# Kernel tuning notes

Hardware: AMD Instinct MI355X
Metric: run time of the kernel (lower is better)

Reference implementation:

```python
import jax, jax.numpy as jnp
import numpy as np

N_STREAMS = 8
DIM = 1024
N_HEADS = 16
HEAD_DIM = DIM // N_HEADS
STREAM_DIM = DIM // N_STREAMS
EPS = 1e-6


def setup_inputs() -> dict:
    key = jax.random.key(0)
    ks = jax.random.split(key, 20)
    B, S, D = 2, 2048, DIM
    inp = {
        "x": jax.random.normal(ks[0], (B, S, D), jnp.float32),
        "rope_cos": jax.random.uniform(ks[1], (S, HEAD_DIM), jnp.float32),
        "rope_sin": jax.random.uniform(ks[2], (S, HEAD_DIM), jnp.float32),
        # DeltaOperator: learned per-channel decay logits
        "delta_decay": jax.random.normal(ks[3], (D,), jnp.float32) * 0.02,
        # gate_proj: Linear(D, 3*n)
        "gate_w": jax.random.normal(ks[4], (3 * N_STREAMS, D), jnp.float32) * 0.02,
        "gate_b": jnp.zeros((3 * N_STREAMS,), jnp.float32),
        "phi_res": jax.random.normal(ks[5], (N_STREAMS, N_STREAMS), jnp.float32) * 0.02,
        "ln1_w": jnp.ones((D,), jnp.float32),
        "ln2_w": jnp.ones((D,), jnp.float32),
        # MLP (StrategicLinear == Linear at inference)
        "w1": jax.random.normal(ks[6], (4 * D, D), jnp.float32) * 0.02,
        "b1": jnp.zeros((4 * D,), jnp.float32),
        "w2": jax.random.normal(ks[7], (D, 4 * D), jnp.float32) * 0.02,
        "b2": jnp.zeros((D,), jnp.float32),
        # nn.MultiheadAttention params
        "in_proj_w": jax.random.normal(ks[8], (3 * D, D), jnp.float32) * 0.02,
        "in_proj_b": jnp.zeros((3 * D,), jnp.float32),
        "out_w": jax.random.normal(ks[9], (D, D), jnp.float32) * 0.02,
        "out_b": jnp.zeros((D,), jnp.float32),
    }
    return inp


def delta_operator(x, decay_logits):
    # out_t = x_t - s_{t-1};  s_t = beta*s_{t-1} + (1-beta)*x_t  (per-channel EMA delta)
    beta = jax.nn.sigmoid(decay_logits)  # [D]

    def step(s, xt):
        out = xt - s
        s_new = beta * s + (1.0 - beta) * xt
        return s_new, out

    xT = jnp.swapaxes(x, 0, 1)  # [S,B,D]
    s0 = jnp.zeros_like(xT[0])
    _, ysT = jax.lax.scan(step, s0, xT)
    return jnp.swapaxes(ysT, 0, 1)  # [B,S,D]


def rms_norm(x, w):
    var = jnp.mean(x * x, axis=-1, keepdims=True)
    return x * jax.lax.rsqrt(var + EPS) * w


def sinkhorn_knopp(phi, iterations=15):
    K = jnp.exp(phi)
    for _ in range(iterations):
        K = K / jnp.sum(K, axis=1, keepdims=True)
        K = K / jnp.sum(K, axis=0, keepdims=True)
    return K


def causal_mha(x, in_proj_w, in_proj_b, out_w, out_b):
    B, S, D = x.shape
    qkv = x @ in_proj_w.T + in_proj_b  # [B,S,3D]
    q, k, v = jnp.split(qkv, 3, axis=-1)
    def heads(t):
        return t.reshape(B, S, N_HEADS, HEAD_DIM).transpose(0, 2, 1, 3)  # [B,H,S,hd]
    q, k, v = heads(q), heads(k), heads(v)
    scores = jnp.einsum("bhqd,bhkd->bhqk", q, k) / jnp.sqrt(jnp.float32(HEAD_DIM))
    mask = jnp.tril(jnp.ones((S, S), bool))
    scores = jnp.where(mask, scores, jnp.float32(-1e9))
    attn = jax.nn.softmax(scores, axis=-1)
    o = jnp.einsum("bhqk,bhkd->bhqd", attn, v)
    o = o.transpose(0, 2, 1, 3).reshape(B, S, D)
    return o @ out_w.T + out_b


def reference(x, rope_cos, rope_sin, delta_decay, gate_w, gate_b, phi_res,
              ln1_w, ln2_w, w1, b1, w2, b2, in_proj_w, in_proj_b, out_w, out_b):
    B, S, D = x.shape
    n = N_STREAMS
    x_delta = delta_operator(x, delta_decay)
    x_state = jnp.mean(x_delta, axis=1)  # [B,D]
    gates = x_state @ gate_w.T + gate_b  # [B,3n]
    g_res = jax.nn.sigmoid(gates[:, 2 * n:])[:, None, :, None]  # [B,1,n,1]
    H_res = sinkhorn_knopp(phi_res, 15)
    x_streams = x_delta.reshape(B, S, n, STREAM_DIM)
    # (x_perm @ H.T).permute back == einsum over stream axis
    mhc_out = jnp.einsum("bsnd,mn->bsmd", x_streams * g_res, H_res).reshape(B, S, D)
    normed = rms_norm(x_delta, ln1_w)
    attn_out = causal_mha(normed, in_proj_w, in_proj_b, out_w, out_b)
    normed2 = rms_norm(x_delta + attn_out, ln2_w)
    h = jax.nn.gelu(normed2 @ w1.T + b1, approximate=False)
    ffn_out = h @ w2.T + b2
    return x_delta + attn_out + ffn_out + mhc_out
```

## Files before the change

kernel.cpp:

```cpp
#include <hip/hip_runtime.h>
#include <hip/hip_bf16.h>
#include <math.h>

#define BB 2
#define SS 2048
#define DDIM 1024
#define NHEAD 16
#define NSTR 8
#define SDIMC 128
#define NCH 16
#define CLEN 128
#define EPSV 1e-6f

using bf16 = __hip_bfloat16;
typedef __attribute__((ext_vector_type(8))) __bf16 bf8;
typedef __attribute__((ext_vector_type(4))) float f4;

__device__ __forceinline__ bf16 f2b(float v) { return __float2bfloat16(v); }
__device__ __forceinline__ bf8 ld8(const bf16* p) { return *(const bf8*)p; }
__device__ __forceinline__ f4 MFMA(bf8 a, bf8 b, f4 c) {
  return __builtin_amdgcn_mfma_f32_16x16x32_bf16(a, b, c, 0, 0, 0);
}
__device__ __forceinline__ float sigm(float x) { return 1.0f / (1.0f + expf(-x)); }
__device__ __forceinline__ float fexp2(float x) { return __builtin_amdgcn_exp2f(x); }

__device__ __forceinline__ void glds16(bf16* l, const bf16* g) {
  __builtin_amdgcn_global_load_lds(
      (const __attribute__((address_space(1))) unsigned int*)g,
      (__attribute__((address_space(3))) unsigned int*)l, 16, 0, 0);
}

__global__ __launch_bounds__(256) void cvt_all(const float* __restrict__ ipw,
                                               const float* __restrict__ ow,
                                               const float* __restrict__ w1,
                                               const float* __restrict__ w2,
                                               bf16* __restrict__ WIPW,
                                               bf16* __restrict__ WOW,
                                               bf16* __restrict__ W1B,
                                               bf16* __restrict__ W2B) {
  const int S1 = 3 * DDIM * DDIM, S2 = S1 + DDIM * DDIM,
            S3 = S2 + 4 * DDIM * DDIM;
  int i4 = (blockIdx.x * 256 + threadIdx.x) * 4;
  const float* src;
  bf16* dst;
  int off;
  if (i4 < S1)      { src = ipw; dst = WIPW; off = i4; }
  else if (i4 < S2) { src = ow;  dst = WOW;  off = i4 - S1; }
  else if (i4 < S3) { src = w1;  dst = W1B;  off = i4 - S2; }
  else              { src = w2;  dst = W2B;  off = i4 - S3; }
  float4 v = *(const float4*)(src + off);
  dst[off]     = f2b(v.x);
  dst[off + 1] = f2b(v.y);
  dst[off + 2] = f2b(v.z);
  dst[off + 3] = f2b(v.w);
}

__global__ __launch_bounds__(256) void delta_passA(const float* __restrict__ x,
                                                   const float* __restrict__ decay,
                                                   float* __restrict__ SA) {
  int idx = blockIdx.x * 256 + threadIdx.x;
  int d = idx % DDIM;
  int c = (idx / DDIM) % NCH;
  int b = idx / (DDIM * NCH);
  float beta = sigm(decay[d]);
  float omb = 1.0f - beta;
  const float* xp = x + ((size_t)(b * SS + c * CLEN)) * DDIM + d;
  float s = 0.0f;
  for (int j = 0; j < CLEN; j++) {
    float xv = xp[(size_t)j * DDIM];
    s = beta * s + omb * xv;
  }
  SA[idx] = s;
}

__global__ __launch_bounds__(256) void delta_passB(const float* __restrict__ SA,
                                                   const float* __restrict__ decay,
                                                   float* __restrict__ SIN) {
  int idx = blockIdx.x * 256 + threadIdx.x;
  int d = idx % DDIM;
  int b = idx / DDIM;
  float beta = sigm(decay[d]);
  float p = beta;
  for (int i = 0; i < 7; i++) p *= p;
  float s = 0.0f;
  for (int c = 0; c < NCH; c++) {
    SIN[(b * NCH + c) * DDIM + d] = s;
    s = p * s + SA[(b * NCH + c) * DDIM + d];
  }
}

__global__ __launch_bounds__(256) void delta_passC(const float* __restrict__ x,
                                                   const float* __restrict__ decay,
                                                   const float* __restrict__ SIN,
                                                   float* __restrict__ XD,
                                                   float* __restrict__ SA) {
  int idx = blockIdx.x * 256 + threadIdx.x;
  int d = idx % DDIM;
  int c = (idx / DDIM) % NCH;
  int b = idx / (DDIM * NCH);
  float beta = sigm(decay[d]);
  float omb = 1.0f - beta;
  const float* xp = x + ((size_t)(b * SS + c * CLEN)) * DDIM + d;
  float* xdp = XD + ((size_t)(b * SS + c * CLEN)) * DDIM + d;
  float s = SIN[idx];
  float sum = 0.0f;
  for (int j = 0; j < CLEN; j++) {
    float xv = xp[(size_t)j * DDIM];
    float o = xv - s;
    xdp[(size_t)j * DDIM] = o;
    sum += o;
    s = beta * s + omb * xv;
  }
  SA[idx] = sum;
}

__global__ __launch_bounds__(1024) void gates_sinkhorn(const float* __restrict__ SA,
                                                       const float* __restrict__ gw,
                                                       const float* __restrict__ gb,
                                                       const float* __restrict__ phi,
                                                       float* __restrict__ gres,
                                                       float* __restrict__ hres) {
  int tid = threadIdx.x;
  int wave = tid >> 6, lane = tid & 63;
  int b = wave >> 3, j = wave & 7;
  float acc = 0.0f;
  for (int d = lane; d < DDIM; d += 64) {
    float xs = 0.0f;
    for (int c = 0; c < NCH; c++) xs += SA[(b * NCH + c) * DDIM + d];
    xs *= (1.0f / (float)SS);
    acc += xs * gw[(2 * NSTR + j) * DDIM + d];
  }
  for (int off = 32; off > 0; off >>= 1) acc += __shfl_down(acc, off);
  if (lane == 0) gres[b * NSTR + j] = sigm(acc + gb[2 * NSTR + j]);
  __syncthreads();
  if (tid == 0) {
    float Km[8][8];
    for (int i = 0; i < 8; i++)
      for (int jj = 0; jj < 8; jj++) Km[i][jj] = expf(phi[i * 8 + jj]);
    for (int it = 0; it < 15; it++) {
      for (int i = 0; i < 8; i++) {
        float rs = 0.0f;
        for (int jj = 0; jj < 8; jj++) rs += Km[i][jj];
        float inv = 1.0f / rs;
        for (int jj = 0; jj < 8; jj++) Km[i][jj] *= inv;
      }
      for (int jj = 0; jj < 8; jj++) {
        float cs = 0.0f;
        for (int i = 0; i < 8; i++) cs += Km[i][jj];
        float inv = 1.0f / cs;
        for (int i = 0; i < 8; i++) Km[i][jj] *= inv;
      }
    }
    for (int i = 0; i < 8; i++)
      for (int jj = 0; jj < 8; jj++) hres[i * 8 + jj] = Km[i][jj];
  }
}

__global__ __launch_bounds__(256) void rmsnorm_k(const float* __restrict__ in,
                                                 const float* __restrict__ w,
                                                 bf16* __restrict__ out) {
  int row = blockIdx.x;
  const float* r = in + (size_t)row * DDIM;
  int tid = threadIdx.x;
  float ss = 0.0f;
  for (int i = tid; i < DDIM; i += 256) {
    float v = r[i];
    ss += v * v;
  }
  for (int off = 32; off > 0; off >>= 1) ss += __shfl_down(ss, off);
  __shared__ float red[4];
  if ((tid & 63) == 0) red[tid >> 6] = ss;
  __syncthreads();
  float tot = red[0] + red[1] + red[2] + red[3];
  float sc = rsqrtf(tot / (float)DDIM + EPSV);
  bf16* o = out + (size_t)row * DDIM;
  for (int i = tid; i < DDIM; i += 256) o[i] = f2b(r[i] * sc * w[i]);
}

template <int ODT, int EPI>
__global__ __launch_bounds__(256) void gemm_lds(const bf16* __restrict__ A,
                                                const bf16* __restrict__ W,
                                                const float* __restrict__ bias,
                                                const float* __restrict__ res,
                                                void* __restrict__ outp,
                                                int M, int N, int K) {
  __shared__ bf16 As[128 * 32];
  __shared__ bf16 Bs[128 * 32];
  int tid = threadIdx.x;
  int lane = tid & 63, wv = tid >> 6;
  int ml = lane & 15, quad = lane >> 4;
  int wr = wv >> 1, wc = wv & 1;
  int m0 = blockIdx.x * 128, n0 = blockIdx.y * 128;
  f4 acc[4][4] = {};
  for (int k0 = 0; k0 < K; k0 += 32) {
#pragma unroll
    for (int it = 0; it < 2; it++) {
      int c = it * 256 + tid;
      int row = c >> 2, kc = (c & 3) * 8;
      glds16(&As[c * 8], A + (size_t)(m0 + row) * K + k0 + kc);
      glds16(&Bs[c * 8], W + (size_t)(n0 + row) * K + k0 + kc);
    }
    __syncthreads();
    bf8 af[4], bfr[4];
#pragma unroll
    for (int mi = 0; mi < 4; mi++)
      af[mi] = ld8(&As[(wr * 64 + mi * 16 + ml) * 32 + quad * 8]);
#pragma unroll
    for (int ni = 0; ni < 4; ni++)
      bfr[ni] = ld8(&Bs[(wc * 64 + ni * 16 + ml) * 32 + quad * 8]);
#pragma unroll
    for (int mi = 0; mi < 4; mi++)
#pragma unroll
      for (int ni = 0; ni < 4; ni++)
        acc[mi][ni] = MFMA(af[mi], bfr[ni], acc[mi][ni]);
    __syncthreads();
  }
#pragma unroll
  for (int mi = 0; mi < 4; mi++)
#pragma unroll
    for (int ni = 0; ni < 4; ni++)
#pragma unroll
      for (int r = 0; r < 4; r++) {
        int row = m0 + wr * 64 + mi * 16 + quad * 4 + r;
        int col = n0 + wc * 64 + ni * 16 + ml;
        size_t idx = (size_t)row * N + col;
        float v = acc[mi][ni][r] + bias[col];
        if (EPI == 1) v = 0.5f * v * (1.0f + erff(v * 0.70710678118654752f));
        if (EPI == 2) v += res[idx];
        if (ODT == 1) ((bf16*)outp)[idx] = f2b(v);
        else ((float*)outp)[idx] = v;
      }
}

__global__ __launch_bounds__(256) void gemm_part2(const bf16* __restrict__ A,
                                                  const bf16* __restrict__ W,
                                                  float* __restrict__ P0,
                                                  float* __restrict__ P1,
                                                  int M, int N, int KS, int LDK) {
  __shared__ bf16 As[128 * 32];
  __shared__ bf16 Bs[128 * 32];
  int tid = threadIdx.x;
  int lane = tid & 63, wv = tid >> 6;
  int ml = lane & 15, quad = lane >> 4;
  int wr = wv >> 1, wc = wv & 1;
  int m0 = blockIdx.x * 128, n0 = blockIdx.y * 128;
  const bf16* Ab = A + blockIdx.z * KS;
  const bf16* Wb = W + blockIdx.z * KS;
  float* P = blockIdx.z ? P1 : P0;
  f4 acc[4][4] = {};
  for (int k0 = 0; k0 < KS; k0 += 32) {
#pragma unroll
    for (int it = 0; it < 2; it++) {
      int c = it * 256 + tid;
      int row = c >> 2, kc = (c & 3) * 8;
      glds16(&As[c * 8], Ab + (size_t)(m0 + row) * LDK + k0 + kc);
      glds16(&Bs[c * 8], Wb + (size_t)(n0 + row) * LDK + k0 + kc);
    }
    __syncthreads();
    bf8 af[4], bfr[4];
#pragma unroll
    for (int mi = 0; mi < 4; mi++)
      af[mi] = ld8(&As[(wr * 64 + mi * 16 + ml) * 32 + quad * 8]);
#pragma unroll
    for (int ni = 0; ni < 4; ni++)
      bfr[ni] = ld8(&Bs[(wc * 64 + ni * 16 + ml) * 32 + quad * 8]);
#pragma unroll
    for (int mi = 0; mi < 4; mi++)
#pragma unroll
      for (int ni = 0; ni < 4; ni++)
        acc[mi][ni] = MFMA(af[mi], bfr[ni], acc[mi][ni]);
    __syncthreads();
  }
#pragma unroll
  for (int mi = 0; mi < 4; mi++)
#pragma unroll
    for (int ni = 0; ni < 4; ni++)
#pragma unroll
      for (int r = 0; r < 4; r++) {
        int row = m0 + wr * 64 + mi * 16 + quad * 4 + r;
        int col = n0 + wc * 64 + ni * 16 + ml;
        P[(size_t)row * N + col] = acc[mi][ni][r];
      }
}

template <int ODT, int EPI>
__global__ __launch_bounds__(256) void gemm_lds64(const bf16* __restrict__ A,
                                                  const bf16* __restrict__ W,
                                                  const float* __restrict__ bias,
                                                  const float* __restrict__ res,
                                                  void* __restrict__ outp,
                                                  int M, int N, int K) {
  __shared__ bf16 As[64 * 32];
  __shared__ bf16 Bs[128 * 32];
  int tid = threadIdx.x;
  int lane = tid & 63, wv = tid >> 6;
  int ml = lane & 15, quad = lane >> 4;
  int wr = wv & 1, wc = wv >> 1;
  int m0 = blockIdx.x * 64, n0 = blockIdx.y * 128;
  f4 acc[2][4] = {};
  for (int k0 = 0; k0 < K; k0 += 32) {
    {
      int c = tid;
      int row = c >> 2, kc = (c & 3) * 8;
      glds16(&As[c * 8], A + (size_t)(m0 + row) * K + k0 + kc);
    }
#pragma unroll
    for (int it = 0; it < 2; it++) {
      int c = it * 256 + tid;
      int row = c >> 2, kc = (c & 3) * 8;
      glds16(&Bs[c * 8], W + (size_t)(n0 + row) * K + k0 + kc);
    }
    __syncthreads();
    bf8 af[2], bfr[4];
#pragma unroll
    for (int mi = 0; mi < 2; mi++)
      af[mi] = ld8(&As[(wr * 32 + mi * 16 + ml) * 32 + quad * 8]);
#pragma unroll
    for (int ni = 0; ni < 4; ni++)
      bfr[ni] = ld8(&Bs[(wc * 64 + ni * 16 + ml) * 32 + quad * 8]);
#pragma unroll
    for (int mi = 0; mi < 2; mi++)
#pragma unroll
      for (int ni = 0; ni < 4; ni++)
        acc[mi][ni] = MFMA(af[mi], bfr[ni], acc[mi][ni]);
    __syncthreads();
  }
#pragma unroll
  for (int mi = 0; mi < 2; mi++)
#pragma unroll
    for (int ni = 0; ni < 4; ni++)
#pragma unroll
      for (int r = 0; r < 4; r++) {
        int row = m0 + wr * 32 + mi * 16 + quad * 4 + r;
        int col = n0 + wc * 64 + ni * 16 + ml;
        size_t idx = (size_t)row * N + col;
        float v = acc[mi][ni][r] + bias[col];
        if (EPI == 1) v = 0.5f * v * (1.0f + erff(v * 0.70710678118654752f));
        if (EPI == 2) v += res[idx];
        if (ODT == 1) ((bf16*)outp)[idx] = f2b(v);
        else ((float*)outp)[idx] = v;
      }
}

__global__ __launch_bounds__(256) void vtrans(const bf16* __restrict__ qkv,
                                              bf16* __restrict__ VT) {
  int bid = blockIdx.x;
  int st = bid % (SS / 64);
  int h = (bid / (SS / 64)) % NHEAD;
  int b = bid / ((SS / 64) * NHEAD);
  __shared__ bf16 tile[64][65];
  int s0 = st * 64;
  int tid = threadIdx.x;
  for (int it = 0; it < 16; it++) {
    int sl = it * 4 + (tid >> 6), dl = tid & 63;
    tile[sl][dl] = qkv[(size_t)(b * SS + s0 + sl) * (3 * DDIM) + 2 * DDIM + h * 64 + dl];
  }
  __syncthreads();
  for (int it = 0; it < 16; it++) {
    int dl = it * 4 + (tid >> 6), sl = tid & 63;
    VT[((size_t)(b * NHEAD + h) * 64 + dl) * SS + s0 + sl] = tile[sl][dl];
  }
}

__device__ __forceinline__ void phase_tile(int kt, int q0, int nkt,
                                           const bf8* qf, f4* oacc,
                                           float* m_r, float* l_r,
                                           const bf16* __restrict__ Ks,
                                           const bf16* __restrict__ Vs,
                                           bf16 (*pl)[72], int ml, int quad) {
  if (kt >= nkt) return;
  const float SC = 0.125f * 1.44269504089f;
  int k0 = kt * 64;
  f4 sacc[4] = {{0,0,0,0},{0,0,0,0},{0,0,0,0},{0,0,0,0}};
#pragma unroll
  for (int kk = 0; kk < 2; kk++)
#pragma unroll
    for (int c = 0; c < 4; c++) {
      int chunk = ((c * 16 + ml) << 3) + ((kk * 4 + quad) ^ (ml & 7));
      bf8 kf = ld8(&Ks[chunk * 8]);
      sacc[c] = MFMA(qf[kk], kf, sacc[c]);
    }
  float sv[4][4];
#pragma unroll
  for (int c = 0; c < 4; c++)
#pragma unroll
    for (int r = 0; r < 4; r++) sv[c][r] = sacc[c][r] * SC;
  if (kt == nkt - 1) {
#pragma unroll
    for (int c = 0; c < 4; c++)
#pragma unroll
      for (int r = 0; r < 4; r++) {
        int qi = q0 + quad * 4 + r;
        int kj = k0 + c * 16 + ml;
        if (kj > qi) sv[c][r] = -1e9f;
      }
  }
  float alpha[4];
#pragma unroll
  for (int r = 0; r < 4; r++) {
    float mx = fmaxf(fmaxf(sv[0][r], sv[1][r]), fmaxf(sv[2][r], sv[3][r]));
#pragma unroll
    for (int off = 1; off < 16; off <<= 1) mx = fmaxf(mx, __shfl_xor(mx, off));
    float mn = fmaxf(m_r[r], mx);
    float rs = 0.0f;
#pragma unroll
    for (int c = 0; c < 4; c++) {
      float p = fexp2(sv[c][r] - mn);
      sv[c][r] = p;
      rs += p;
    }
#pragma unroll
    for (int off = 1; off < 16; off <<= 1) rs += __shfl_xor(rs, off);
    alpha[r] = fexp2(m_r[r] - mn);
    l_r[r] = l_r[r] * alpha[r] + rs;
    m_r[r] = mn;
  }
#pragma unroll
  for (int c = 0; c < 4; c++)
#pragma unroll
    for (int r = 0; r < 4; r++) oacc[c][r] *= alpha[r];
#pragma unroll
  for (int c = 0; c < 4; c++)
#pragma unroll
    for (int r = 0; r < 4; r++)
      pl[quad * 4 + r][c * 16 + ml] = f2b(sv[c][r]);
  bf8 pf[2];
#pragma unroll
  for (int kk = 0; kk < 2; kk++) pf[kk] = ld8(&pl[ml][kk * 32 + quad * 8]);
#pragma unroll
  for (int c = 0; c < 4; c++)
#pragma unroll
    for (int kk = 0; kk < 2; kk++) {
      int chunk = ((c * 16 + ml) << 3) + ((kk * 4 + quad) ^ (ml & 7));
      bf8 vf = ld8(&Vs[chunk * 8]);
      oacc[c] = MFMA(pf[kk], vf, oacc[c]);
    }
}

__global__ __launch_bounds__(256) void flash_attn(const bf16* __restrict__ qkv,
                                                  const bf16* __restrict__ VT,
                                                  bf16* __restrict__ obuf) {
  int bid = blockIdx.x;
  int blk = bid & 15;
  int h = (bid >> 4) & 15;
  int b = bid >> 8;
  int tid = threadIdx.x;
  int wv = tid >> 6, lane = tid & 63;
  int ml = lane & 15, quad = lane >> 4;
  int idx0 = blk * 4 + wv;
  int idx1 = 127 - idx0;
  int q0a = idx0 * 16, q0b = idx1 * 16;
  int nkt0 = blk + 1;
  int nkt1 = 32 - blk;
  int maxn = nkt1;

  __shared__ __align__(16) bf16 Ks[64 * 64];
  __shared__ __align__(16) bf16 Vs[64 * 64];
  __shared__ __align__(16) bf16 plds[4][16][72];
  bf16 (*pl)[72] = plds[wv];

  bf8 qfa[2], qfb[2];
#pragma unroll
  for (int kk = 0; kk < 2; kk++) {
    qfa[kk] = ld8(qkv + (size_t)(b * SS + q0a + ml) * (3 * DDIM) + h * 64 + kk * 32 + quad * 8);
    qfb[kk] = ld8(qkv + (size_t)(b * SS + q0b + ml) * (3 * DDIM) + h * 64 + kk * 32 + quad * 8);
  }
  f4 oacca[4] = {{0,0,0,0},{0,0,0,0},{0,0,0,0},{0,0,0,0}};
  f4 oaccb[4] = {{0,0,0,0},{0,0,0,0},{0,0,0,0},{0,0,0,0}};
  float ma[4], la[4], mb[4], lb[4];
#pragma unroll
  for (int r = 0; r < 4; r++) {
    ma[r] = -1e30f; la[r] = 0.0f;
    mb[r] = -1e30f; lb[r] = 0.0f;
  }

  const bf16* kglob = qkv + (size_t)b * SS * (3 * DDIM) + DDIM + h * 64;
  const bf16* vglob = VT + (size_t)(b * NHEAD + h) * 64 * SS;

  for (int kt = 0; kt < maxn; kt++) {
    int k0 = kt * 64;
#pragma unroll
    for (int it = 0; it < 2; it++) {
      int lam = it * 256 + tid;
      int row = lam >> 3;
      int ch = (lam & 7) ^ (row & 7);
      glds16(&Ks[lam * 8], kglob + (size_t)(k0 + row) * (3 * DDIM) + ch * 8);
      glds16(&Vs[lam * 8], vglob + (size_t)row * SS + k0 + ch * 8);
    }
    __syncthreads();
    phase_tile(kt, q0a, nkt0, qfa, oacca, ma, la, Ks, Vs, pl, ml, quad);
    phase_tile(kt, q0b, nkt1, qfb, oaccb, mb, lb, Ks, Vs, pl, ml, quad);
    __syncthreads();
  }
#pragma unroll
  for (int c = 0; c < 4; c++)
#pragma unroll
    for (int r = 0; r < 4; r++) {
      int rowa = q0a + quad * 4 + r;
      int rowb = q0b + quad * 4 + r;
      obuf[(size_t)(b * SS + rowa) * DDIM + h * 64 + c * 16 + ml] =
          f2b(oacca[c][r] / la[r]);
      obuf[(size_t)(b * SS + rowb) * DDIM + h * 64 + c * 16 + ml] =
          f2b(oaccb[c][r] / lb[r]);
    }
}

__global__ __launch_bounds__(256) void final_k(const float* __restrict__ y,
                                               const float* __restrict__ P0,
                                               const float* __restrict__ P1,
                                               const float* __restrict__ bias,
                                               const float* __restrict__ xd,
                                               const float* __restrict__ hres,
                                               const float* __restrict__ gres,
                                               float* __restrict__ out) {
  int row = blockIdx.x;
  int b = row / SS;
  int tid = threadIdx.x;
  __shared__ float cf[8][8];
  if (tid < 64) cf[tid >> 3][tid & 7] = hres[tid] * gres[b * NSTR + (tid & 7)];
  __syncthreads();
  const float* yr = y + (size_t)row * DDIM;
  const float* p0 = P0 + (size_t)row * DDIM;
  const float* p1 = P1 + (size_t)row * DDIM;
  const float* xr = xd + (size_t)row * DDIM;
  float* o = out + (size_t)row * DDIM;
  for (int i = tid; i < DDIM; i += 256) {
    int m = i >> 7, dd = i & 127;
    float acc = yr[i] + p0[i] + p1[i] + bias[i];
#pragma unroll
    for (int n = 0; n < 8; n++) acc += cf[m][n] * xr[n * SDIMC + dd];
    o[i] = acc;
  }
}

extern "C" void kernel_launch(void* const* d_in, const int* in_sizes, int n_in,
                              void* d_out, int out_size, void* d_ws, size_t ws_size,
                              hipStream_t stream) {
  const float* x     = (const float*)d_in[0];
  const float* decay = (const float*)d_in[3];
  const float* gw    = (const float*)d_in[4];
  const float* gb    = (const float*)d_in[5];
  const float* phi   = (const float*)d_in[6];
  const float* ln1   = (const float*)d_in[7];
  const float* ln2   = (const float*)d_in[8];
  const float* w1    = (const float*)d_in[9];
  const float* b1    = (const float*)d_in[10];
  const float* w2    = (const float*)d_in[11];
  const float* b2    = (const float*)d_in[12];
  const float* ipw   = (const float*)d_in[13];
  const float* ipb   = (const float*)d_in[14];
  const float* ow    = (const float*)d_in[15];
  const float* obs   = (const float*)d_in[16];
  float* out = (float*)d_out;

  const size_t MB = 1048576ull;
  char* wsp = (char*)d_ws;
  float* SA   = (float*)(wsp);
  float* SIN  = (float*)(wsp + 131072ull);
  float* GRES = (float*)(wsp + 262144ull);
  float* HRES = (float*)(wsp + 262208ull);
  float* XD   = (float*)(wsp + 1 * MB);
  float* AO   = (float*)(wsp + 17 * MB);
  bf16*  NORM = (bf16*)(wsp + 33 * MB);
  bf16*  OB   = (bf16*)(wsp + 41 * MB);
  bf16*  QKV  = (bf16*)(wsp + 49 * MB);
  bf16*  VT   = (bf16*)(wsp + 73 * MB);
  bf16*  HB   = (bf16*)(wsp + 49 * MB);
  bf16*  WIPW = (bf16*)(wsp + 81 * MB);
  bf16*  WOW  = (bf16*)(wsp + 87 * MB);
  bf16*  W1B  = (bf16*)(wsp + 89 * MB);
  bf16*  W2B  = (bf16*)(wsp + 97 * MB);
  float* PK0  = (float*)(wsp + 33 * MB);
  float* PK1  = (float*)(wsp + 81 * MB);

  cvt_all<<<dim3(12 * DDIM * DDIM / 1024), dim3(256), 0, stream>>>(
      ipw, ow, w1, w2, WIPW, WOW, W1B, W2B);

  delta_passA<<<dim3(BB * NCH * DDIM / 256), dim3(256), 0, stream>>>(x, decay, SA);
  delta_passB<<<dim3(BB * DDIM / 256), dim3(256), 0, stream>>>(SA, decay, SIN);
  delta_passC<<<dim3(BB * NCH * DDIM / 256), dim3(256), 0, stream>>>(x, decay, SIN, XD, SA);
  gates_sinkhorn<<<dim3(1), dim3(1024), 0, stream>>>(SA, gw, gb, phi, GRES, HRES);
  rmsnorm_k<<<dim3(BB * SS), dim3(256), 0, stream>>>(XD, ln1, NORM);
  gemm_lds<1, 0><<<dim3(32, 24), dim3(256), 0, stream>>>(NORM, WIPW, ipb, nullptr,
                                                         QKV, BB * SS, 3 * DDIM, DDIM);
  vtrans<<<dim3(BB * NHEAD * (SS / 64)), dim3(256), 0, stream>>>(QKV, VT);
  flash_attn<<<dim3(BB * NHEAD * 16), dim3(256), 0, stream>>>(QKV, VT, OB);
  gemm_lds64<0, 2><<<dim3(64, 8), dim3(256), 0, stream>>>(OB, WOW, obs, XD,
                                                          AO, BB * SS, DDIM, DDIM);
  rmsnorm_k<<<dim3(BB * SS), dim3(256), 0, stream>>>(AO, ln2, NORM);
  gemm_lds<1, 1><<<dim3(32, 32), dim3(256), 0, stream>>>(NORM, W1B, b1, nullptr,
                                                         HB, BB * SS, 4 * DDIM, DDIM);
  gemm_part2<<<dim3(32, 8, 2), dim3(256), 0, stream>>>(HB, W2B, PK0, PK1,
                                                       BB * SS, DDIM, 2 * DDIM, 4 * DDIM);
  final_k<<<dim3(BB * SS), dim3(256), 0, stream>>>(AO, PK0, PK1, b2, XD,
                                                   HRES, GRES, out);
}
```

Measured before the change: 471.4 us.

## Double-buffer LDS tiles in GEMMs and flash attention, use fast GELU

All three GEMM kernels and the flash-attention kernel now use two LDS buffers. The next K-tile is issued with global_load_lds before the MFMAs on the current tile, which removes one barrier per iteration and hides global-load latency behind compute. The exact erff GELU is replaced by an Abramowitz-Stegun polynomial erf using hardware rcp and exp2, accurate to roughly 1e-7. The weight-conversion kernel now does one vectorized 4-wide bf16 store instead of four scalar stores. The cost is double the LDS footprint per block, which can lower occupancy.

```diff
diff --git a/kernel.cpp b/kernel.cpp
--- a/kernel.cpp
+++ b/kernel.cpp
@@ -14,6 +14,7 @@
 
 using bf16 = __hip_bfloat16;
 typedef __attribute__((ext_vector_type(8))) __bf16 bf8;
+typedef __attribute__((ext_vector_type(4))) __bf16 bf4v;
 typedef __attribute__((ext_vector_type(4))) float f4;
 
 __device__ __forceinline__ bf16 f2b(float v) { return __float2bfloat16(v); }
@@ -23,6 +24,17 @@
 }
 __device__ __forceinline__ float sigm(float x) { return 1.0f / (1.0f + expf(-x)); }
 __device__ __forceinline__ float fexp2(float x) { return __builtin_amdgcn_exp2f(x); }
+
+__device__ __forceinline__ float gelu_f(float v) {
+  float x = v * 0.70710678118654752f;
+  float ax = fabsf(x);
+  float t = __builtin_amdgcn_rcpf(1.0f + 0.3275911f * ax);
+  float p = ((((1.061405429f * t - 1.453152027f) * t + 1.421413741f) * t
+              - 0.284496736f) * t + 0.254829592f) * t;
+  float e = 1.0f - p * fexp2(-ax * ax * 1.4426950408889634f);
+  e = copysignf(e, x);
+  return 0.5f * v * (1.0f + e);
+}
 
 __device__ __forceinline__ void glds16(bf16* l, const bf16* g) {
   __builtin_amdgcn_global_load_lds(
@@ -49,10 +61,9 @@
   else if (i4 < S3) { src = w1;  dst = W1B;  off = i4 - S2; }
   else              { src = w2;  dst = W2B;  off = i4 - S3; }
   float4 v = *(const float4*)(src + off);
-  dst[off]     = f2b(v.x);
-  dst[off + 1] = f2b(v.y);
-  dst[off + 2] = f2b(v.z);
-  dst[off + 3] = f2b(v.w);
+  bf4v o;
+  o[0] = (__bf16)v.x; o[1] = (__bf16)v.y; o[2] = (__bf16)v.z; o[3] = (__bf16)v.w;
+  *(bf4v*)(dst + off) = o;
 }
 
 __global__ __launch_bounds__(256) void delta_passA(const float* __restrict__ x,
@@ -184,36 +195,56 @@
                                                 const float* __restrict__ res,
                                                 void* __restrict__ outp,
                                                 int M, int N, int K) {
-  __shared__ bf16 As[128 * 32];
-  __shared__ bf16 Bs[128 * 32];
+  __shared__ bf16 As[2][128 * 32];
+  __shared__ bf16 Bs[2][128 * 32];
   int tid = threadIdx.x;
   int lane = tid & 63, wv = tid >> 6;
   int ml = lane & 15, quad = lane >> 4;
   int wr = wv >> 1, wc = wv & 1;
   int m0 = blockIdx.x * 128, n0 = blockIdx.y * 128;
+  const bf16* ga[2];
+  const bf16* gb[2];
+  int lofs[2];
+#pragma unroll
+  for (int it = 0; it < 2; it++) {
+    int c = it * 256 + tid;
+    int row = c >> 2, kc = (c & 3) * 8;
+    ga[it] = A + (size_t)(m0 + row) * K + kc;
+    gb[it] = W + (size_t)(n0 + row) * K + kc;
+    lofs[it] = c * 8;
+  }
+#pragma unroll
+  for (int it = 0; it < 2; it++) {
+    glds16(&As[0][lofs[it]], ga[it]);
+    glds16(&Bs[0][lofs[it]], gb[it]);
+  }
   f4 acc[4][4] = {};
-  for (int k0 = 0; k0 < K; k0 += 32) {
-#pragma unroll
-    for (int it = 0; it < 2; it++) {
-      int c = it * 256 + tid;
-      int row = c >> 2, kc = (c & 3) * 8;
-      glds16(&As[c * 8], A + (size_t)(m0 + row) * K + k0 + kc);
-      glds16(&Bs[c * 8], W + (size_t)(n0 + row) * K + k0 + kc);
-    }
-    __syncthreads();
+  int nk = K >> 5;
+  int cur = 0;
+  __syncthreads();
+  for (int t = 0; t < nk; t++) {
+    if (t + 1 < nk) {
+      int ko = (t + 1) * 32;
+#pragma unroll
+      for (int it = 0; it < 2; it++) {
+        glds16(&As[cur ^ 1][lofs[it]], ga[it] + ko);
+        glds16(&Bs[cur ^ 1][lofs[it]], gb[it] + ko);
+      }
+    }
     bf8 af[4], bfr[4];
 #pragma unroll
     for (int mi = 0; mi < 4; mi++)
-      af[mi] = ld8(&As[(wr * 64 + mi * 16 + ml) * 32 + quad * 8]);
+      af[mi] = ld8(&As[cur][(wr * 64 + mi * 16 + ml) * 32 + quad * 8]);
 #pragma unroll
     for (int ni = 0; ni < 4; ni++)
-      bfr[ni] = ld8(&Bs[(wc * 64 + ni * 16 + ml) * 32 + quad * 8]);
+      bfr[ni] = ld8(&Bs[cur][(wc * 64 + ni * 16 + ml) * 32 + quad * 8]);
 #pragma unroll
     for (int mi = 0; mi < 4; mi++)
 #pragma unroll
       for (int ni = 0; ni < 4; ni++)
         acc[mi][ni] = MFMA(af[mi], bfr[ni], acc[mi][ni]);
     __syncthreads();
+    cur ^= 1;
   }
 #pragma unroll
   for (int mi = 0; mi < 4; mi++)
@@ -225,7 +256,7 @@
         int col = n0 + wc * 64 + ni * 16 + ml;
         size_t idx = (size_t)row * N + col;
         float v = acc[mi][ni][r] + bias[col];
-        if (EPI == 1) v = 0.5f * v * (1.0f + erff(v * 0.70710678118654752f));
+        if (EPI == 1) v = gelu_f(v);
         if (EPI == 2) v += res[idx];
         if (ODT == 1) ((bf16*)outp)[idx] = f2b(v);
         else ((float*)outp)[idx] = v;
@@ -237,8 +268,8 @@
                                                   float* __restrict__ P0,
                                                   float* __restrict__ P1,
                                                   int M, int N, int KS, int LDK) {
-  __shared__ bf16 As[128 * 32];
-  __shared__ bf16 Bs[128 * 32];
+  __shared__ bf16 As[2][128 * 32];
+  __shared__ bf16 Bs[2][128 * 32];
   int tid = threadIdx.x;
   int lane = tid & 63, wv = tid >> 6;
   int ml = lane & 15, quad = lane >> 4;
@@ -247,29 +278,49 @@
   const bf16* Ab = A + blockIdx.z * KS;
   const bf16* Wb = W + blockIdx.z * KS;
   float* P = blockIdx.z ? P1 : P0;
+  const bf16* ga[2];
+  const bf16* gb[2];
+  int lofs[2];
+#pragma unroll
+  for (int it = 0; it < 2; it++) {
+    int c = it * 256 + tid;
+    int row = c >> 2, kc = (c & 3) * 8;
+    ga[it] = Ab + (size_t)(m0 + row) * LDK + kc;
+    gb[it] = Wb + (size_t)(n0 + row) * LDK + kc;
+    lofs[it] = c * 8;
+  }
+#pragma unroll
+  for (int it = 0; it < 2; it++) {
+    glds16(&As[0][lofs[it]], ga[it]);
+    glds16(&Bs[0][lofs[it]], gb[it]);
+  }
   f4 acc[4][4] = {};
-  for (int k0 = 0; k0 < KS; k0 += 32) {
-#pragma unroll
-    for (int it = 0; it < 2; it++) {
-      int c = it * 256 + tid;
-      int row = c >> 2, kc = (c & 3) * 8;
-      glds16(&As[c * 8], Ab + (size_t)(m0 + row) * LDK + k0 + kc);
-      glds16(&Bs[c * 8], Wb + (size_t)(n0 + row) * LDK + k0 + kc);
-    }
-    __syncthreads();
+  int nk = KS >> 5;
+  int cur = 0;
+  __syncthreads();
+  for (int t = 0; t < nk; t++) {
+    if (t + 1 < nk) {
+      int ko = (t + 1) * 32;
+#pragma unroll
+      for (int it = 0; it < 2; it++) {
+        glds16(&As[cur ^ 1][lofs[it]], ga[it] + ko);
+        glds16(&Bs[cur ^ 1][lofs[it]], gb[it] + ko);
+      }
+    }
     bf8 af[4], bfr[4];
 #pragma unroll
     for (int mi = 0; mi < 4; mi++)
-      af[mi] = ld8(&As[(wr * 64 + mi * 16 + ml) * 32 + quad * 8]);
+      af[mi] = ld8(&As[cur][(wr * 64 + mi * 16 + ml) * 32 + quad * 8]);
 #pragma unroll
     for (int ni = 0; ni < 4; ni++)
-      bfr[ni] = ld8(&Bs[(wc * 64 + ni * 16 + ml) * 32 + quad * 8]);
+      bfr[ni] = ld8(&Bs[cur][(wc * 64 + ni * 16 + ml) * 32 + quad * 8]);
 #pragma unroll
     for (int mi = 0; mi < 4; mi++)
 #pragma unroll
       for (int ni = 0; ni < 4; ni++)
         acc[mi][ni] = MFMA(af[mi], bfr[ni], acc[mi][ni]);
     __syncthreads();
+    cur ^= 1;
   }
 #pragma unroll
   for (int mi = 0; mi < 4; mi++)
@@ -290,40 +341,57 @@
                                                   const float* __restrict__ res,
                                                   void* __restrict__ outp,
                                                   int M, int N, int K) {
-  __shared__ bf16 As[64 * 32];
-  __shared__ bf16 Bs[128 * 32];
+  __shared__ bf16 As[2][64 * 32];
+  __shared__ bf16 Bs[2][128 * 32];
   int tid = threadIdx.x;
   int lane = tid & 63, wv = tid >> 6;
   int ml = lane & 15, quad = lane >> 4;
   int wr = wv & 1, wc = wv >> 1;
   int m0 = blockIdx.x * 64, n0 = blockIdx.y * 128;
+  const bf16* gaA;
+  const bf16* gb[2];
+  int lofA, lofs[2];
+  {
+    int c = tid;
+    int row = c >> 2, kc = (c & 3) * 8;
+    gaA = A + (size_t)(m0 + row) * K + kc;
+    lofA = c * 8;
+  }
+#pragma unroll
+  for (int it = 0; it < 2; it++) {
+    int c = it * 256 + tid;
+    int row = c >> 2, kc = (c & 3) * 8;
+    gb[it] = W + (size_t)(n0 + row) * K + kc;
+    lofs[it] = c * 8;
+  }
+  glds16(&As[0][lofA], gaA);
+#pragma unroll
+  for (int it = 0; it < 2; it++) glds16(&Bs[0][lofs[it]], gb[it]);
   f4 acc[2][4] = {};
-  for (int k0 = 0; k0 < K; k0 += 32) {
-    {
-      int c = tid;
-      int row = c >> 2, kc = (c & 3) * 8;
-      glds16(&As[c * 8], A + (size_t)(m0 + row) * K + k0 + kc);
-    }
-#pragma unroll
-    for (int it = 0; it < 2; it++) {
-      int c = it * 256 + tid;
-      int row = c >> 2, kc = (c & 3) * 8;
-      glds16(&Bs[c * 8], W + (size_t)(n0 + row) * K + k0 + kc);
-    }
-    __syncthreads();
+  int nk = K >> 5;
+  int cur = 0;
+  __syncthreads();
+  for (int t = 0; t < nk; t++) {
+    if (t + 1 < nk) {
+      int ko = (t + 1) * 32;
+      glds16(&As[cur ^ 1][lofA], gaA + ko);
+#pragma unroll
+      for (int it = 0; it < 2; it++) glds16(&Bs[cur ^ 1][lofs[it]], gb[it] + ko);
+    }
     bf8 af[2], bfr[4];
 #pragma unroll
     for (int mi = 0; mi < 2; mi++)
-      af[mi] = ld8(&As[(wr * 32 + mi * 16 + ml) * 32 + quad * 8]);
+      af[mi] = ld8(&As[cur][(wr * 32 + mi * 16 + ml) * 32 + quad * 8]);
 #pragma unroll
     for (int ni = 0; ni < 4; ni++)
-      bfr[ni] = ld8(&Bs[(wc * 64 + ni * 16 + ml) * 32 + quad * 8]);
+      bfr[ni] = ld8(&Bs[cur][(wc * 64 + ni * 16 + ml) * 32 + quad * 8]);
 #pragma unroll
     for (int mi = 0; mi < 2; mi++)
 #pragma unroll
       for (int ni = 0; ni < 4; ni++)
         acc[mi][ni] = MFMA(af[mi], bfr[ni], acc[mi][ni]);
     __syncthreads();
+    cur ^= 1;
   }
 #pragma unroll
   for (int mi = 0; mi < 2; mi++)
@@ -335,7 +403,7 @@
         int col = n0 + wc * 64 + ni * 16 + ml;
         size_t idx = (size_t)row * N + col;
         float v = acc[mi][ni][r] + bias[col];
-        if (EPI == 1) v = 0.5f * v * (1.0f + erff(v * 0.70710678118654752f));
+        if (EPI == 1) v = gelu_f(v);
         if (EPI == 2) v += res[idx];
         if (ODT == 1) ((bf16*)outp)[idx] = f2b(v);
         else ((float*)outp)[idx] = v;
@@ -454,8 +522,8 @@
   int nkt1 = 32 - blk;
   int maxn = nkt1;
 
-  __shared__ __align__(16) bf16 Ks[64 * 64];
-  __shared__ __align__(16) bf16 Vs[64 * 64];
+  __shared__ __align__(16) bf16 Ks[2][64 * 64];
+  __shared__ __align__(16) bf16 Vs[2][64 * 64];
   __shared__ __align__(16) bf16 plds[4][16][72];
   bf16 (*pl)[72] = plds[wv];
 
@@ -477,20 +545,32 @@
   const bf16* kglob = qkv + (size_t)b * SS * (3 * DDIM) + DDIM + h * 64;
   const bf16* vglob = VT + (size_t)(b * NHEAD + h) * 64 * SS;
 
+#pragma unroll
+  for (int it = 0; it < 2; it++) {
+    int lam = it * 256 + tid;
+    int row = lam >> 3;
+    int ch = (lam & 7) ^ (row & 7);
+    glds16(&Ks[0][lam * 8], kglob + (size_t)row * (3 * DDIM) + ch * 8);
+    glds16(&Vs[0][lam * 8], vglob + (size_t)row * SS + ch * 8);
+  }
+  __syncthreads();
+  int cur = 0;
   for (int kt = 0; kt < maxn; kt++) {
-    int k0 = kt * 64;
-#pragma unroll
-    for (int it = 0; it < 2; it++) {
-      int lam = it * 256 + tid;
-      int row = lam >> 3;
-      int ch = (lam & 7) ^ (row & 7);
-      glds16(&Ks[lam * 8], kglob + (size_t)(k0 + row) * (3 * DDIM) + ch * 8);
-      glds16(&Vs[lam * 8], vglob + (size_t)row * SS + k0 + ch * 8);
-    }
+    if (kt + 1 < maxn) {
+      int k0n = (kt + 1) * 64;
+#pragma unroll
+      for (int it = 0; it < 2; it++) {
+        int lam = it * 256 + tid;
+        int row = lam >> 3;
+        int ch = (lam & 7) ^ (row & 7);
+        glds16(&Ks[cur ^ 1][lam * 8], kglob + (size_t)(k0n + row) * (3 * DDIM) + ch * 8);
+        glds16(&Vs[cur ^ 1][lam * 8], vglob + (size_t)row * SS + k0n + ch * 8);
+      }
+    }
+    phase_tile(kt, q0a, nkt0, qfa, oacca, ma, la, Ks[cur], Vs[cur], pl, ml, quad);
+    phase_tile(kt, q0b, nkt1, qfb, oaccb, mb, lb, Ks[cur], Vs[cur], pl, ml, quad);
     __syncthreads();
-    phase_tile(kt, q0a, nkt0, qfa, oacca, ma, la, Ks, Vs, pl, ml, quad);
-    phase_tile(kt, q0b, nkt1, qfb, oaccb, mb, lb, Ks, Vs, pl, ml, quad);
-    __syncthreads();
+    cur ^= 1;
   }
 #pragma unroll
   for (int c = 0; c < 4; c++)
```

Result: faster. 443.6 us (-5.9%).
